# Kernel optimization log

Measured on AMD Instinct MI355X. Metric: run time of the kernel, lower is better.

## Reference

```python
import jax, jax.numpy as jnp
import numpy as np

H = 16        # head_nums
DN = 128      # qk_nope_head_dim
DR = 64       # qk_rope_head_dim
DV = 128      # v_head_dim
QLR = 1536    # q_lora_rank
KVLR = 512    # kv_lora_rank
HID = 2048    # hidden_dim
THETA = 10000.0
EPS = 1e-6


def _rms(x, w):
    return x * jax.lax.rsqrt(jnp.mean(x * x, axis=-1, keepdims=True) + EPS) * w


def _reorder(x):
    # replicates view(b,h,s,d//2,2).transpose(4,3).reshape: [x0,x2,...,x1,x3,...]
    return jnp.concatenate([x[..., 0::2], x[..., 1::2]], axis=-1)


def _rotate_half(x):
    h = x.shape[-1] // 2
    return jnp.concatenate([-x[..., h:], x[..., :h]], axis=-1)


def setup_inputs() -> dict:
    key = jax.random.key(0)
    ks = jax.random.split(key, 7)
    B, S = 1, 2048

    def w(k, i, o):
        return jax.random.normal(k, (i, o), jnp.float32) * (i ** -0.5)

    return {
        "x": jax.random.normal(ks[0], (B, S, HID), jnp.float32),
        "Wq_down": w(ks[1], HID, QLR),
        "q_norm_w": jnp.ones((QLR,), jnp.float32),
        "Wq_up": w(ks[2], QLR, H * (DN + DR)),
        "Wkv_down": w(ks[3], HID, KVLR + DR),
        "kv_norm_w": jnp.ones((KVLR,), jnp.float32),
        "Wkv_up": w(ks[4], KVLR, H * (DN + DV)),
        "Wo": w(ks[5], HID, HID),
        "position": jnp.broadcast_to(jnp.arange(S, dtype=jnp.int32)[None], (B, S)),
        "mask": jnp.tril(jnp.ones((S, S), bool))[None, None],  # causal [1,1,S,S]
    }


def reference(x, Wq_down, q_norm_w, Wq_up, Wkv_down, kv_norm_w, Wkv_up, Wo, position, mask):
    B, S, _ = x.shape
    # low-rank Q path: down-proj -> RMSNorm -> up-proj -> [B,H,S,DN+DR]
    q = _rms(x @ Wq_down, q_norm_w) @ Wq_up
    q = q.reshape(B, S, H, DN + DR).transpose(0, 2, 1, 3)
    q_nope, q_rope = q[..., :DN], q[..., DN:]
    # latent KV path
    ckv = x @ Wkv_down
    c, k_rope = ckv[..., :KVLR], ckv[..., KVLR:]
    c = _rms(c, kv_norm_w)
    kv = (c @ Wkv_up).reshape(B, S, H, DN + DV).transpose(0, 2, 1, 3)
    k_nope, v = kv[..., :DN], kv[..., DN:]
    k_rope = k_rope[:, None]  # [B,1,S,DR] shared across heads
    # rotary tables
    inv_freq = 1.0 / (THETA ** (jnp.arange(0, DR, 2, dtype=jnp.float32) / DR))
    t = jnp.arange(S, dtype=jnp.float32)
    emb = jnp.concatenate([jnp.outer(t, inv_freq)] * 2, axis=-1)  # [S,DR]
    cos = jnp.cos(emb)[position][:, None]  # [B,1,S,DR]
    sin = jnp.sin(emb)[position][:, None]
    qr, kr = _reorder(q_rope), _reorder(k_rope)
    q_rot = qr * cos + _rotate_half(qr) * sin
    k_rot = kr * cos + _rotate_half(kr) * sin
    q_state = jnp.concatenate([q_nope, q_rot], axis=-1)              # [B,H,S,DN+DR]
    k_state = jnp.concatenate(
        [k_nope, jnp.broadcast_to(k_rot, (B, H, S, DR))], axis=-1)   # [B,H,S,DN+DR]
    scores = jnp.einsum('bhsd,bhtd->bhst', q_state, k_state) / np.float32(np.sqrt(DV))
    scores = jnp.where(mask, scores, -jnp.inf)
    att = jax.nn.softmax(scores, axis=-1)
    out = jnp.einsum('bhst,bhtd->bhsd', att, v)
    out = out.transpose(0, 2, 1, 3).reshape(B, S, H * DV)
    return out @ Wo
```

## Files before the change

kernel.cpp:

```cpp
#include <hip/hip_runtime.h>
#include <hip/hip_bf16.h>
#include <cstddef>

#define H 16
#define DN 128
#define DR 64
#define DV 128
#define QLR 1536
#define KVLR 512
#define HID 2048
#define SLEN 2048
#define EPS 1e-6f
#define SCALE 0.08838834764831845f
#define QK_SCALE (0.08838834764831845f * 1.4426950408889634f)

typedef __attribute__((ext_vector_type(8))) short short8;
typedef __attribute__((ext_vector_type(4))) float f32x4;
typedef unsigned short u16;

__device__ __forceinline__ u16 f2bf(float f) {
    __hip_bfloat16 h = __float2bfloat16(f);
    return __builtin_bit_cast(u16, h);
}
__device__ __forceinline__ float b2f(u16 v) {
    return __bfloat162float(__builtin_bit_cast(__hip_bfloat16, v));
}
__device__ __forceinline__ unsigned pack2(float a, float b) {
    return (unsigned)f2bf(a) | ((unsigned)f2bf(b) << 16);
}

__device__ __forceinline__ void tcast_block(
    const float* __restrict__ W, u16* __restrict__ Wt,
    int K, int N, int nx, float scale, int b, float (*T)[65])
{
    const int tid = threadIdx.x;
    const int bx = b % nx, by = b / nx;
    const int n0 = bx * 64, k0 = by * 64;
    const bool inb = (n0 < N);
    {
        int r = tid >> 4, c4 = (tid & 15) * 4;
        #pragma unroll
        for (int rr = 0; rr < 4; ++rr) {
            int row = rr * 16 + r;
            float4 v = inb ? *reinterpret_cast<const float4*>(W + (size_t)(k0 + row) * N + n0 + c4)
                           : make_float4(0.f, 0.f, 0.f, 0.f);
            T[row][c4] = v.x * scale; T[row][c4 + 1] = v.y * scale;
            T[row][c4 + 2] = v.z * scale; T[row][c4 + 3] = v.w * scale;
        }
    }
    __syncthreads();
    {
        int n = tid >> 2, kq = (tid & 3) * 16;
        unsigned u[8];
        #pragma unroll
        for (int jj = 0; jj < 8; ++jj)
            u[jj] = pack2(T[kq + 2 * jj][n], T[kq + 2 * jj + 1][n]);
        u16* dst = Wt + (size_t)(n0 + n) * K + k0 + kq;
        *reinterpret_cast<uint4*>(dst)     = make_uint4(u[0], u[1], u[2], u[3]);
        *reinterpret_cast<uint4*>(dst + 8) = make_uint4(u[4], u[5], u[6], u[7]);
    }
}

__global__ __launch_bounds__(256) void prep_all(
    const float* __restrict__ x, u16* __restrict__ xb,
    const float* __restrict__ Wqd, const float* __restrict__ Wkvd,
    u16* __restrict__ BtF)
{
    const int tid = threadIdx.x;
    if (blockIdx.x < 2048) {
        size_t base = ((size_t)blockIdx.x * 256 + tid) * 8;
        float4 v0 = *reinterpret_cast<const float4*>(x + base);
        float4 v1 = *reinterpret_cast<const float4*>(x + base + 4);
        union { short8 s; unsigned u[4]; } p;
        p.u[0] = pack2(v0.x, v0.y); p.u[1] = pack2(v0.z, v0.w);
        p.u[2] = pack2(v1.x, v1.y); p.u[3] = pack2(v1.z, v1.w);
        *reinterpret_cast<short8*>(xb + base) = p.s;
        return;
    }
    __shared__ float T[64][65];
    int b = blockIdx.x - 2048;
    if (b < 768) tcast_block(Wqd, BtF, 2048, 1536, 24, 1.0f, b, T);
    else         tcast_block(Wkvd, BtF + (size_t)1536 * 2048, 2048, 576, 10, 1.0f, b - 768, T);
}

__device__ __forceinline__ void stage6(const char* const* gb, const unsigned* srcOff,
                                       const int* ldsBase, u16* smemBuf, unsigned koff)
{
    #pragma unroll
    for (int j = 0; j < 6; ++j)
        __builtin_amdgcn_global_load_lds(
            (const __attribute__((address_space(1))) unsigned int*)(gb[j] + srcOff[j] + koff),
            (__attribute__((address_space(3))) unsigned int*)(smemBuf + ldsBase[j]),
            16, 0, 0);
}

template<bool BF16OUT>
__device__ __forceinline__ void gemm_core64(
    const u16* __restrict__ A, const u16* __restrict__ Bt, void* __restrict__ Cv,
    int N, int K, int m0, int n0, u16 (*smem)[12288])
{
    const int tid = threadIdx.x, lane = tid & 63, w = tid >> 6;
    const int colk = lane & 15, grp16 = (lane >> 4) * 16;
    const size_t Kb = (size_t)K * 2;

    const char* gb[6];
    unsigned srcOff[6];
    int ldsBase[6];
    #pragma unroll
    for (int j = 0; j < 6; ++j) {
        int c = w * 6 + j;
        bool isA = (c < 8);
        int cc = isA ? c : c - 8;
        int o = cc * 1024 + lane * 16;
        int u = o ^ (((o >> 7) & 7) << 4);
        int row = u >> 7, kbyte = u & 127;
        gb[j] = isA ? (const char*)A : (const char*)Bt;
        srcOff[j] = (unsigned)((size_t)(isA ? m0 + row : n0 + row) * Kb + kbyte);
        ldsBase[j] = isA ? cc * 512 : 4096 + cc * 512;
    }

    const int wc = w * 32;
    int aoff[8], boff[4];
    #pragma unroll
    for (int ks = 0; ks < 2; ++ks) {
        #pragma unroll
        for (int i = 0; i < 4; ++i) {
            int ra = i * 16 + colk;
            int oa = ra * 128 + ks * 64 + grp16;
            aoff[ks * 4 + i] = oa ^ ((ra & 7) << 4);
        }
        #pragma unroll
        for (int jj = 0; jj < 2; ++jj) {
            int rb = wc + jj * 16 + colk;
            int ob = rb * 128 + ks * 64 + grp16;
            boff[ks * 2 + jj] = (ob ^ ((rb & 7) << 4)) + 8192;
        }
    }

    f32x4 acc[4][2];
    #pragma unroll
    for (int i = 0; i < 4; ++i)
        #pragma unroll
        for (int j = 0; j < 2; ++j) acc[i][j] = (f32x4){0.f, 0.f, 0.f, 0.f};

    const int NT = K >> 6;
    stage6(gb, srcOff, ldsBase, &smem[0][0], 0);
    __syncthreads();
    int cur = 0;
    for (int t = 0; t < NT; ++t) {
        if (t + 1 < NT) stage6(gb, srcOff, ldsBase, &smem[cur ^ 1][0], (unsigned)(t + 1) * 128);
        const char* base = (const char*)&smem[cur][0];
        #pragma unroll
        for (int ks = 0; ks < 2; ++ks) {
            short8 af[4], bfr[2];
            #pragma unroll
            for (int i = 0; i < 4; ++i) af[i] = *reinterpret_cast<const short8*>(base + aoff[ks * 4 + i]);
            #pragma unroll
            for (int jj = 0; jj < 2; ++jj) bfr[jj] = *reinterpret_cast<const short8*>(base + boff[ks * 2 + jj]);
            __builtin_amdgcn_s_setprio(1);
            #pragma unroll
            for (int i = 0; i < 4; ++i)
                #pragma unroll
                for (int jj = 0; jj < 2; ++jj)
                    acc[i][jj] = __builtin_amdgcn_mfma_f32_16x16x32_bf16(af[i], bfr[jj], acc[i][jj], 0, 0, 0);
            __builtin_amdgcn_s_setprio(0);
        }
        __syncthreads();
        cur ^= 1;
    }

    #pragma unroll
    for (int i = 0; i < 4; ++i) {
        int grow0 = m0 + i * 16 + (grp16 >> 2);
        #pragma unroll
        for (int jj = 0; jj < 2; ++jj) {
            int gcol = n0 + wc + jj * 16 + colk;
            if (gcol < N) {
                #pragma unroll
                for (int r = 0; r < 4; ++r) {
                    float v2 = acc[i][jj][r];
                    if (BF16OUT) ((u16*)Cv)[(size_t)(grow0 + r) * N + gcol] = f2bf(v2);
                    else         ((float*)Cv)[(size_t)(grow0 + r) * N + gcol] = v2;
                }
            }
        }
    }
}

__device__ __forceinline__ void xcd_map(int orig, int nwg, int nby, int& bx, int& by)
{
    int xcd = orig & 7, o8 = orig >> 3;
    int qq = nwg >> 3, rr = nwg & 7;
    int v = (xcd < rr ? xcd * (qq + 1) : rr * (qq + 1) + (xcd - rr) * qq) + o8;
    bx = v / nby; by = v - bx * nby;
}

__global__ __launch_bounds__(256) void gemm_down_fused(
    const u16* __restrict__ xb, const u16* __restrict__ BtF, float* __restrict__ fC,
    const float* __restrict__ Wqu, const float* __restrict__ Wkvu, const float* __restrict__ Wo,
    u16* __restrict__ Wqu_t, u16* __restrict__ Wkvu_t, u16* __restrict__ Wo_t)
{
    __shared__ u16 smem[2][12288];
    if (blockIdx.x < 544) {
        int bx, by;
        xcd_map(blockIdx.x, 544, 32, bx, by);
        gemm_core64<false>(xb, BtF, fC, 2112, 2048, by * 64, bx * 128, smem);
        return;
    }
    float (*T)[65] = reinterpret_cast<float(*)[65]>(&smem[0][0]);
    int b = blockIdx.x - 544;
    if (b < 1152)      tcast_block(Wqu,  Wqu_t,  1536, 3072, 48, QK_SCALE, b, T);
    else if (b < 1664) tcast_block(Wkvu, Wkvu_t, 512,  4096, 64, 1.0f, b - 1152, T);
    else               tcast_block(Wo,   Wo_t,   2048, 2048, 32, 1.0f, b - 1664, T);
}

__global__ __launch_bounds__(256) void gemm_dual(
    const u16* __restrict__ Aq, const u16* __restrict__ Bq, u16* __restrict__ Cq,
    const u16* __restrict__ Ak, const u16* __restrict__ Bk, u16* __restrict__ Ck)
{
    __shared__ u16 smem[2][12288];
    int b = blockIdx.x;
    const u16 *A, *Bt; u16* C; int N, K, nwg;
    if (b < 768) { A = Aq; Bt = Bq; C = Cq; N = 3072; K = 1536; nwg = 768; }
    else { b -= 768; A = Ak; Bt = Bk; C = Ck; N = 4096; K = 512; nwg = 1024; }
    int bx, by;
    xcd_map(b, nwg, 32, bx, by);
    gemm_core64<true>(A, Bt, C, N, K, by * 64, bx * 128, smem);
}

__global__ __launch_bounds__(256) void gemm_wo(
    const u16* __restrict__ A, const u16* __restrict__ Bt, float* __restrict__ C)
{
    __shared__ u16 smem[2][12288];
    int bx, by;
    xcd_map(blockIdx.x, 512, 32, bx, by);
    gemm_core64<false>(A, Bt, C, 2048, 2048, by * 64, bx * 128, smem);
}

__global__ __launch_bounds__(256) void rmsnorm2_bf16(
    const float* __restrict__ fC, const float* __restrict__ qw,
    const float* __restrict__ kvw, u16* __restrict__ qdb, u16* __restrict__ ckvb)
{
    const int row = blockIdx.x, tid = threadIdx.x;
    const float* p = fC + (size_t)row * 2112;
    float ssq = 0.f, ssk = 0.f;
    for (int i = tid * 4; i < 1536; i += 1024) {
        float4 v = *reinterpret_cast<const float4*>(p + i);
        ssq += v.x * v.x + v.y * v.y + v.z * v.z + v.w * v.w;
    }
    if (tid < 128) {
        float4 v = *reinterpret_cast<const float4*>(p + 1536 + tid * 4);
        ssk = v.x * v.x + v.y * v.y + v.z * v.z + v.w * v.w;
    }
    __shared__ float wsq[4], wsk[4];
    int lane = tid & 63, wv = tid >> 6;
    #pragma unroll
    for (int off = 32; off; off >>= 1) {
        ssq += __shfl_down(ssq, off);
        ssk += __shfl_down(ssk, off);
    }
    if (lane == 0) { wsq[wv] = ssq; wsk[wv] = ssk; }
    __syncthreads();
    if (tid == 0) {
        wsq[0] = rsqrtf((wsq[0] + wsq[1] + wsq[2] + wsq[3]) / 1536.f + EPS);
        wsk[0] = rsqrtf((wsk[0] + wsk[1] + wsk[2] + wsk[3]) / 512.f + EPS);
    }
    __syncthreads();
    float scq = wsq[0], sck = wsk[0];
    for (int i = tid * 4; i < 1536; i += 1024) {
        float4 v = *reinterpret_cast<const float4*>(p + i);
        float4 g = *reinterpret_cast<const float4*>(qw + i);
        *reinterpret_cast<uint2*>(qdb + (size_t)row * 1536 + i) =
            make_uint2(pack2(v.x * scq * g.x, v.y * scq * g.y),
                       pack2(v.z * scq * g.z, v.w * scq * g.w));
    }
    if (tid < 128) {
        int i = tid * 4;
        float4 v = *reinterpret_cast<const float4*>(p + 1536 + i);
        float4 g = *reinterpret_cast<const float4*>(kvw + i);
        *reinterpret_cast<uint2*>(ckvb + (size_t)row * 512 + i) =
            make_uint2(pack2(v.x * sck * g.x, v.y * sck * g.y),
                       pack2(v.z * sck * g.z, v.w * sck * g.w));
    }
}

__global__ __launch_bounds__(256) void rope_vtrans(
    u16* __restrict__ q, const float* __restrict__ krsrc, int krStride,
    u16* __restrict__ krot, const u16* __restrict__ kvbf, u16* __restrict__ vtb)
{
    const int tid = threadIdx.x;
    if (blockIdx.x < 2048) {
        const int s = blockIdx.x;
        __shared__ float cs[32], sn[32];
        if (tid < 32) {
            float inv = powf(10000.0f, -(float)tid / 32.0f);
            float ang = (float)s * inv;
            cs[tid] = cosf(ang); sn[tid] = sinf(ang);
        }
        __syncthreads();
        float ev[2], ov[2]; int hh[2], ii[2];
        #pragma unroll
        for (int it = 0; it < 2; ++it) {
            int pidx = tid + it * 256;
            int h = pidx >> 5, i = pidx & 31;
            hh[it] = h; ii[it] = i;
            const u16* base = q + (size_t)s * 3072 + h * 192 + 128;
            ev[it] = b2f(base[2 * i]); ov[it] = b2f(base[2 * i + 1]);
        }
        __syncthreads();
        #pragma unroll
        for (int it = 0; it < 2; ++it) {
            int h = hh[it], i = ii[it];
            u16* base = q + (size_t)s * 3072 + h * 192 + 128;
            base[i]      = f2bf(ev[it] * cs[i] - ov[it] * sn[i]);
            base[32 + i] = f2bf(ov[it] * cs[i] + ev[it] * sn[i]);
        }
        if (tid < 32) {
            int i = tid;
            float e = krsrc[(size_t)s * krStride + 2 * i];
            float o = krsrc[(size_t)s * krStride + 2 * i + 1];
            krot[(size_t)s * 64 + i]      = f2bf(e * cs[i] - o * sn[i]);
            krot[(size_t)s * 64 + 32 + i] = f2bf(o * cs[i] + e * sn[i]);
        }
        return;
    }
    const int bid = blockIdx.x - 2048;
    const int h = bid & 15, rem = bid >> 4;
    const int st = rem & 31, dt = rem >> 5;
    __shared__ u16 T[64][72];
    #pragma unroll
    for (int it = 0; it < 2; ++it) {
        int c = it * 256 + tid;
        int r = c >> 3, c8 = (c & 7) * 8;
        short8 v = *reinterpret_cast<const short8*>(
            kvbf + ((size_t)(st * 64 + r) * 16 + h) * 256 + 128 + dt * 64 + c8);
        *reinterpret_cast<short8*>(&T[r][c8]) = v;
    }
    __syncthreads();
    #pragma unroll
    for (int it = 0; it < 2; ++it) {
        int c = it * 256 + tid;
        int d = c >> 3, s8 = (c & 7) * 8;
        union { short8 s; u16 e[8]; } o;
        #pragma unroll
        for (int j = 0; j < 8; ++j) o.e[j] = T[s8 + j][d];
        *reinterpret_cast<short8*>(
            vtb + ((size_t)(h * 128 + dt * 64 + d)) * 2048 + st * 64 + s8) = o.s;
    }
}

__global__ __launch_bounds__(256, 2) void attn_chunk(
    const u16* __restrict__ qbf,
    const u16* __restrict__ kvbf,
    const u16* __restrict__ krot,
    const u16* __restrict__ vtb,
    u16* __restrict__ outb,
    u16* __restrict__ partAcc,
    float* __restrict__ partML)
{
    const int bid = blockIdx.x;
    const int xcd = bid & 7, slot = bid >> 3;
    const int h = xcd + 8 * (slot & 1);
    const int r80 = 79 - (slot >> 1);
    int qb, ch, S, poff;
    if (r80 < 8)       { qb = r80;                 ch = 0;      S = 1; poff = 0; }
    else if (r80 < 24) { int u = r80 - 8;  qb = 8 + (u >> 1);  ch = u & 1; S = 2; poff = (qb - 8) * 2 + ch; }
    else if (r80 < 48) { int u = r80 - 24; qb = 16 + u / 3;    ch = u % 3; S = 3; poff = 16 + (qb - 16) * 3 + ch; }
    else               { int u = r80 - 48; qb = 24 + (u >> 2); ch = u & 3; S = 4; poff = 40 + (qb - 24) * 4 + ch; }
    const int s0 = qb * 64;
    const int t0 = ch * 8;
    const int t1 = (t0 + 8 < qb + 1) ? (t0 + 8) : (qb + 1);
    const int slotId = h * 72 + poff;
    const int tid = threadIdx.x, lane = tid & 63, w = tid >> 6;
    const int colk = lane & 15, grp = lane >> 4, g8 = grp * 8;

    __shared__ u16 Ks[64 * 192];
    __shared__ u16 Vt[128 * 64];

    const int qg = s0 + w * 16 + colk;

    short8 qreg[6];
    {
        const u16* qp = qbf + ((size_t)qg * H + h) * 192;
        #pragma unroll
        for (int ks = 0; ks < 6; ++ks)
            qreg[ks] = *reinterpret_cast<const short8*>(qp + ks * 32 + g8);
    }

    int kt[6], kslot[6];
    #pragma unroll
    for (int it = 0; it < 6; ++it) {
        int c = it * 256 + tid;
        kt[it] = c / 24; kslot[it] = c % 24;
    }
    int vr[4], vks_[4];
    #pragma unroll
    for (int it = 0; it < 4; ++it) {
        int c = it * 256 + tid;
        vr[it] = c >> 3; vks_[it] = c & 7;
    }

    short8 kreg[6], vregV[4];

    auto issue_loads = [&](int t) {
        #pragma unroll
        for (int it = 0; it < 6; ++it) {
            int gk = t * 64 + kt[it];
            const u16* src = (kslot[it] < 16)
                ? kvbf + ((size_t)gk * H + h) * 256 + kslot[it] * 8
                : krot + (size_t)gk * 64 + (kslot[it] - 16) * 8;
            kreg[it] = *reinterpret_cast<const short8*>(src);
        }
        const u16* vT = vtb + (size_t)h * 128 * 2048 + t * 64;
        #pragma unroll
        for (int it = 0; it < 4; ++it)
            vregV[it] = *reinterpret_cast<const short8*>(
                vT + (size_t)vr[it] * 2048 + vks_[it] * 8);
    };
    auto write_lds = [&]() {
        #pragma unroll
        for (int it = 0; it < 6; ++it) {
            int sl = (kslot[it] & 24) | ((kslot[it] ^ kt[it]) & 7);
            *reinterpret_cast<short8*>(&Ks[kt[it] * 192 + sl * 8]) = kreg[it];
        }
        #pragma unroll
        for (int it = 0; it < 4; ++it)
            *reinterpret_cast<short8*>(
                &Vt[vr[it] * 64 + ((vks_[it] ^ vr[it]) & 7) * 8]) = vregV[it];
    };

    float m_run = -1e30f, l_run = 0.f;
    f32x4 acc_o[8];
    #pragma unroll
    for (int i = 0; i < 8; ++i) acc_o[i] = (f32x4){0.f, 0.f, 0.f, 0.f};

    const int srcA = colk + ((grp & 1) << 5);
    const int srcB = srcA + 16;
    const bool hiSel = (grp >> 1) != 0;

    issue_loads(t0);
    for (int t = t0; t < t1; ++t) {
        __syncthreads();
        write_lds();
        __syncthreads();
        if (t + 1 < t1) issue_loads(t + 1);

        f32x4 sacc[4];
        #pragma unroll
        for (int ct = 0; ct < 4; ++ct) sacc[ct] = (f32x4){0.f, 0.f, 0.f, 0.f};
        __builtin_amdgcn_s_setprio(1);
        #pragma unroll
        for (int ks = 0; ks < 6; ++ks) {
            #pragma unroll
            for (int ct = 0; ct < 4; ++ct) {
                int key = ct * 16 + colk;
                int slotIdx = ks * 4 + grp;
                int sl = (slotIdx & 24) | ((slotIdx ^ key) & 7);
                short8 kf = *reinterpret_cast<const short8*>(&Ks[key * 192 + sl * 8]);
                sacc[ct] = __builtin_amdgcn_mfma_f32_16x16x32_bf16(kf, qreg[ks], sacc[ct], 0, 0, 0);
            }
        }
        __builtin_amdgcn_s_setprio(0);

        if (t == qb) {
            #pragma unroll
            for (int ct = 0; ct < 4; ++ct) {
                int keyb = t * 64 + ct * 16 + 4 * grp;
                #pragma unroll
                for (int r = 0; r < 4; ++r)
                    if (keyb + r > qg) sacc[ct][r] = -1e30f;
            }
        }

        float lmax = fmaxf(fmaxf(fmaxf(sacc[0][0], sacc[0][1]), fmaxf(sacc[0][2], sacc[0][3])),
                           fmaxf(fmaxf(sacc[1][0], sacc[1][1]), fmaxf(sacc[1][2], sacc[1][3])));
        lmax = fmaxf(lmax,
               fmaxf(fmaxf(fmaxf(sacc[2][0], sacc[2][1]), fmaxf(sacc[2][2], sacc[2][3])),
                     fmaxf(fmaxf(sacc[3][0], sacc[3][1]), fmaxf(sacc[3][2], sacc[3][3]))));
        bool need = lmax > m_run + 11.5f;
        if (__any((int)need)) {
            float mx = fmaxf(m_run, lmax);
            mx = fmaxf(mx, __shfl_xor(mx, 16));
            mx = fmaxf(mx, __shfl_xor(mx, 32));
            float f = exp2f(m_run - mx);
            m_run = mx;
            l_run *= f;
            #pragma unroll
            for (int i = 0; i < 8; ++i) {
                acc_o[i][0] *= f; acc_o[i][1] *= f;
                acc_o[i][2] *= f; acc_o[i][3] *= f;
            }
        }

        unsigned pku[8];
        float psum = 0.f;
        #pragma unroll
        for (int ct = 0; ct < 4; ++ct) {
            float p0 = exp2f(sacc[ct][0] - m_run);
            float p1 = exp2f(sacc[ct][1] - m_run);
            float p2 = exp2f(sacc[ct][2] - m_run);
            float p3 = exp2f(sacc[ct][3] - m_run);
            psum += (p0 + p1) + (p2 + p3);
            pku[ct * 2]     = pack2(p0, p1);
            pku[ct * 2 + 1] = pack2(p2, p3);
        }
        l_run += psum;

        __builtin_amdgcn_s_setprio(1);
        #pragma unroll
        for (int ks2 = 0; ks2 < 2; ++ks2) {
            unsigned a0 = __shfl(pku[4 * ks2 + 0], srcA);
            unsigned a1 = __shfl(pku[4 * ks2 + 1], srcA);
            unsigned a2 = __shfl(pku[4 * ks2 + 0], srcB);
            unsigned a3 = __shfl(pku[4 * ks2 + 1], srcB);
            unsigned b0 = __shfl(pku[4 * ks2 + 2], srcA);
            unsigned b1 = __shfl(pku[4 * ks2 + 3], srcA);
            unsigned b2 = __shfl(pku[4 * ks2 + 2], srcB);
            unsigned b3 = __shfl(pku[4 * ks2 + 3], srcB);
            union { short8 s; unsigned u[4]; } bq;
            bq.u[0] = hiSel ? b0 : a0;
            bq.u[1] = hiSel ? b1 : a1;
            bq.u[2] = hiSel ? b2 : a2;
            bq.u[3] = hiSel ? b3 : a3;
            #pragma unroll
            for (int ct = 0; ct < 8; ++ct) {
                int cc = ct * 16 + colk;
                int vsl = ((ks2 * 4 + grp) ^ cc) & 7;
                short8 vb = *reinterpret_cast<const short8*>(&Vt[cc * 64 + vsl * 8]);
                acc_o[ct] = __builtin_amdgcn_mfma_f32_16x16x32_bf16(vb, bq.s, acc_o[ct], 0, 0, 0);
            }
        }
        __builtin_amdgcn_s_setprio(0);
    }

    float l = l_run;
    l += __shfl_xor(l, 16);
    l += __shfl_xor(l, 32);
    const int rloc = w * 16 + colk;
    if (S == 1) {
        float invl = 1.0f / l;
        u16* orow = outb + (size_t)qg * 2048 + h * 128 + 4 * grp;
        #pragma unroll
        for (int ct = 0; ct < 8; ++ct) {
            uint2 pk;
            pk.x = pack2(acc_o[ct][0] * invl, acc_o[ct][1] * invl);
            pk.y = pack2(acc_o[ct][2] * invl, acc_o[ct][3] * invl);
            *reinterpret_cast<uint2*>(orow + ct * 16) = pk;
        }
    } else {
        if (grp == 0) {
            partML[(size_t)slotId * 128 + rloc * 2]     = m_run;
            partML[(size_t)slotId * 128 + rloc * 2 + 1] = l;
        }
        u16* pa = partAcc + (size_t)slotId * 8192 + rloc * 128 + 4 * grp;
        #pragma unroll
        for (int ct = 0; ct < 8; ++ct) {
            uint2 pk;
            pk.x = pack2(acc_o[ct][0], acc_o[ct][1]);
            pk.y = pack2(acc_o[ct][2], acc_o[ct][3]);
            *reinterpret_cast<uint2*>(pa + ct * 16) = pk;
        }
    }
}

__global__ __launch_bounds__(256) void attn_combine(
    const u16* __restrict__ partAcc, const float* __restrict__ partML,
    u16* __restrict__ outb)
{
    const int bid = blockIdx.x;
    const int xcd = bid & 7, s2 = bid >> 3;
    const int h = xcd + 8 * (s2 / 24);
    const int qb = 8 + s2 % 24;
    int S, poff;
    if (qb < 16)      { S = 2; poff = (qb - 8) * 2; }
    else if (qb < 24) { S = 3; poff = 16 + (qb - 16) * 3; }
    else              { S = 4; poff = 40 + (qb - 24) * 4; }
    const int base = h * 72 + poff;
    const int tid = threadIdx.x;
    const int row = tid >> 2, seg = (tid & 3) * 32;

    float mv[4], lv[4];
    float m_g = -1e30f;
    #pragma unroll
    for (int s = 0; s < 4; ++s) {
        bool ok = (s < S);
        mv[s] = ok ? partML[(size_t)(base + s) * 128 + row * 2]     : -1e30f;
        lv[s] = ok ? partML[(size_t)(base + s) * 128 + row * 2 + 1] : 0.f;
        m_g = fmaxf(m_g, mv[s]);
    }
    float l_g = 0.f, wq[4];
    #pragma unroll
    for (int s = 0; s < 4; ++s) { wq[s] = exp2f(mv[s] - m_g); l_g += wq[s] * lv[s]; }
    float inv = 1.f / l_g;
    u16* orow = outb + (size_t)(qb * 64 + row) * 2048 + h * 128 + seg;
    #pragma unroll
    for (int i = 0; i < 8; ++i) {
        float o[4] = {0.f, 0.f, 0.f, 0.f};
        #pragma unroll
        for (int s = 0; s < 4; ++s) {
            if (s < S) {
                ushort4 a = *reinterpret_cast<const ushort4*>(
                    partAcc + (size_t)(base + s) * 8192 + row * 128 + seg + i * 4);
                o[0] += wq[s] * b2f(a.x); o[1] += wq[s] * b2f(a.y);
                o[2] += wq[s] * b2f(a.z); o[3] += wq[s] * b2f(a.w);
            }
        }
        uint2 pk;
        pk.x = pack2(o[0] * inv, o[1] * inv);
        pk.y = pack2(o[2] * inv, o[3] * inv);
        *reinterpret_cast<uint2*>(orow + i * 4) = pk;
    }
}

extern "C" void kernel_launch(void* const* d_in, const int* in_sizes, int n_in,
                              void* d_out, int out_size, void* d_ws, size_t ws_size,
                              hipStream_t stream)
{
    (void)in_sizes; (void)n_in; (void)out_size; (void)ws_size;
    const float* x         = (const float*)d_in[0];
    const float* Wq_down   = (const float*)d_in[1];
    const float* q_norm_w  = (const float*)d_in[2];
    const float* Wq_up     = (const float*)d_in[3];
    const float* Wkv_down  = (const float*)d_in[4];
    const float* kv_norm_w = (const float*)d_in[5];
    const float* Wkv_up    = (const float*)d_in[6];
    const float* Wo        = (const float*)d_in[7];
    float* out = (float*)d_out;

    char* p = (char*)d_ws;
    u16* BtF     = (u16*)p;   p += (size_t)2176 * 2048 * 2;
    u16* Wkvu_t  = (u16*)p;   p += (size_t)4096 * 512  * 2;
    u16* Wo_t    = (u16*)p;   p += (size_t)2048 * 2048 * 2;
    u16* qbuf    = (u16*)p;   p += (size_t)2048 * 3072 * 2;
    u16* ckvb    = (u16*)p;   p += (size_t)2048 * 512  * 2;
    u16* kvbf    = (u16*)p;   p += (size_t)2048 * 4096 * 2;
    u16* krotb   = (u16*)p;   p += (size_t)2048 * 64   * 2;
    char* pool   = p;
    u16* xb      = (u16*)p;   p += (size_t)2048 * 2048 * 2;
    u16* Wqu_t   = (u16*)p;   p += (size_t)3072 * 1536 * 2;
    float* fC    = (float*)p; p += (size_t)2048 * 2112 * 4;
    u16* qdb     = (u16*)p;   p += (size_t)2048 * 1536 * 2;
    u16* attb    = (u16*)BtF;
    u16* partAcc = xb;
    float* partML  = (float*)(partAcc + (size_t)1152 * 8192);
    u16* vtb     = (u16*)(pool + (size_t)20 * 1024 * 1024);

    dim3 blk(256);
    prep_all<<<3136, blk, 0, stream>>>(x, xb, Wq_down, Wkv_down, BtF);

    gemm_down_fused<<<3232, blk, 0, stream>>>(xb, BtF, fC, Wq_up, Wkv_up, Wo,
                                              Wqu_t, Wkvu_t, Wo_t);
    rmsnorm2_bf16<<<2048, blk, 0, stream>>>(fC, q_norm_w, kv_norm_w, qdb, ckvb);
    gemm_dual<<<dim3(1792), blk, 0, stream>>>(qdb, Wqu_t, qbuf, ckvb, Wkvu_t, kvbf);
    rope_vtrans<<<3072, blk, 0, stream>>>(qbuf, fC + 2048, 2112, krotb, kvbf, vtb);

    attn_chunk<<<dim3(1280), blk, 0, stream>>>(qbuf, kvbf, krotb, vtb, attb, partAcc, partML);
    attn_combine<<<dim3(384), blk, 0, stream>>>(partAcc, partML, attb);

    gemm_wo<<<dim3(512), blk, 0, stream>>>(attb, Wo_t, out);
}
```

Measured before the change: 187.7 us.

## Double-buffer attention KV tiles via direct global-to-LDS loads with 32-key tiles

The attention kernel now streams K and V tiles straight from global memory into LDS with global_load_lds, bypassing the register staging copy. Two LDS buffers allow the next tile's load to overlap compute on the current one. Each tile shrinks from 64 keys to 32, which keeps the double buffer within a similar LDS budget and uses a new swizzle. Only one barrier per iteration remains, but there are twice as many iterations, and the smaller tiles give less MFMA work per barrier and per softmax step.

```diff
diff --git a/kernel.cpp b/kernel.cpp
--- a/kernel.cpp
+++ b/kernel.cpp
@@ -368,14 +368,14 @@
     else if (r80 < 48) { int u = r80 - 24; qb = 16 + u / 3;    ch = u % 3; S = 3; poff = 16 + (qb - 16) * 3 + ch; }
     else               { int u = r80 - 48; qb = 24 + (u >> 2); ch = u & 3; S = 4; poff = 40 + (qb - 24) * 4 + ch; }
     const int s0 = qb * 64;
-    const int t0 = ch * 8;
-    const int t1 = (t0 + 8 < qb + 1) ? (t0 + 8) : (qb + 1);
+    const int nt32 = 2 * qb + 2;
+    const int t0 = ch * 16;
+    const int t1 = (t0 + 16 < nt32) ? (t0 + 16) : nt32;
     const int slotId = h * 72 + poff;
     const int tid = threadIdx.x, lane = tid & 63, w = tid >> 6;
     const int colk = lane & 15, grp = lane >> 4, g8 = grp * 8;
 
-    __shared__ u16 Ks[64 * 192];
-    __shared__ u16 Vt[128 * 64];
+    __shared__ u16 smem[2][10240];
 
     const int qg = s0 + w * 16 + colk;
 
@@ -387,47 +387,38 @@
             qreg[ks] = *reinterpret_cast<const short8*>(qp + ks * 32 + g8);
     }
 
-    int kt[6], kslot[6];
-    #pragma unroll
-    for (int it = 0; it < 6; ++it) {
-        int c = it * 256 + tid;
-        kt[it] = c / 24; kslot[it] = c % 24;
-    }
-    int vr[4], vks_[4];
-    #pragma unroll
-    for (int it = 0; it < 4; ++it) {
-        int c = it * 256 + tid;
-        vr[it] = c >> 3; vks_[it] = c & 7;
-    }
-
-    short8 kreg[6], vregV[4];
-
-    auto issue_loads = [&](int t) {
-        #pragma unroll
-        for (int it = 0; it < 6; ++it) {
-            int gk = t * 64 + kt[it];
-            const u16* src = (kslot[it] < 16)
-                ? kvbf + ((size_t)gk * H + h) * 256 + kslot[it] * 8
-                : krot + (size_t)gk * 64 + (kslot[it] - 16) * 8;
-            kreg[it] = *reinterpret_cast<const short8*>(src);
-        }
-        const u16* vT = vtb + (size_t)h * 128 * 2048 + t * 64;
-        #pragma unroll
-        for (int it = 0; it < 4; ++it)
-            vregV[it] = *reinterpret_cast<const short8*>(
-                vT + (size_t)vr[it] * 2048 + vks_[it] * 8);
-    };
-    auto write_lds = [&]() {
-        #pragma unroll
-        for (int it = 0; it < 6; ++it) {
-            int sl = (kslot[it] & 24) | ((kslot[it] ^ kt[it]) & 7);
-            *reinterpret_cast<short8*>(&Ks[kt[it] * 192 + sl * 8]) = kreg[it];
-        }
-        #pragma unroll
-        for (int it = 0; it < 4; ++it)
-            *reinterpret_cast<short8*>(
-                &Vt[vr[it] * 64 + ((vks_[it] ^ vr[it]) & 7) * 8]) = vregV[it];
-    };
+    const char* gbase[5];
+    unsigned curOff[5], strideB[5];
+    int ldsOff[5];
+    #pragma unroll
+    for (int j = 0; j < 5; ++j) {
+        int c = w * 5 + j;
+        if (c < 12) {
+            int o = c * 1024 + lane * 16;
+            int row = o / 384, rem = o % 384, s = rem >> 4;
+            int kslot = (s & 24) | ((s ^ row) & 7);
+            if (kslot < 16) {
+                gbase[j] = (const char*)(kvbf + h * 256);
+                curOff[j] = (unsigned)((row * 4096 + kslot * 8) * 2);
+                strideB[j] = 32 * 4096 * 2;
+            } else {
+                gbase[j] = (const char*)krot;
+                curOff[j] = (unsigned)((row * 64 + (kslot - 16) * 8) * 2);
+                strideB[j] = 32 * 64 * 2;
+            }
+            ldsOff[j] = c * 512;
+        } else {
+            int cc = c - 12;
+            int o = cc * 1024 + lane * 16;
+            int row = o >> 6, s = (o & 63) >> 4;
+            int vks = (s ^ row ^ (row >> 2)) & 3;
+            gbase[j] = (const char*)(vtb + (size_t)h * 128 * 2048);
+            curOff[j] = (unsigned)((row * 2048 + vks * 8) * 2);
+            strideB[j] = 32 * 2;
+            ldsOff[j] = 6144 + cc * 512;
+        }
+        curOff[j] += (unsigned)t0 * strideB[j];
+    }
 
     float m_run = -1e30f, l_run = 0.f;
     f32x4 acc_o[8];
@@ -438,34 +429,53 @@
     const int srcB = srcA + 16;
     const bool hiSel = (grp >> 1) != 0;
 
-    issue_loads(t0);
+    #pragma unroll
+    for (int j = 0; j < 5; ++j) {
+        __builtin_amdgcn_global_load_lds(
+            (const __attribute__((address_space(1))) unsigned int*)(gbase[j] + curOff[j]),
+            (__attribute__((address_space(3))) unsigned int*)(&smem[0][0] + ldsOff[j]),
+            16, 0, 0);
+        curOff[j] += strideB[j];
+    }
+    __syncthreads();
+
+    int buf = 0;
     for (int t = t0; t < t1; ++t) {
-        __syncthreads();
-        write_lds();
-        __syncthreads();
-        if (t + 1 < t1) issue_loads(t + 1);
-
-        f32x4 sacc[4];
-        #pragma unroll
-        for (int ct = 0; ct < 4; ++ct) sacc[ct] = (f32x4){0.f, 0.f, 0.f, 0.f};
+        if (t + 1 < t1) {
+            u16* dst = &smem[buf ^ 1][0];
+            #pragma unroll
+            for (int j = 0; j < 5; ++j) {
+                __builtin_amdgcn_global_load_lds(
+                    (const __attribute__((address_space(1))) unsigned int*)(gbase[j] + curOff[j]),
+                    (__attribute__((address_space(3))) unsigned int*)(dst + ldsOff[j]),
+                    16, 0, 0);
+                curOff[j] += strideB[j];
+            }
+        }
+        const u16* KsB = &smem[buf][0];
+        const u16* VtB = &smem[buf][6144];
+
+        f32x4 sacc[2];
+        sacc[0] = (f32x4){0.f, 0.f, 0.f, 0.f};
+        sacc[1] = (f32x4){0.f, 0.f, 0.f, 0.f};
         __builtin_amdgcn_s_setprio(1);
         #pragma unroll
         for (int ks = 0; ks < 6; ++ks) {
             #pragma unroll
-            for (int ct = 0; ct < 4; ++ct) {
+            for (int ct = 0; ct < 2; ++ct) {
                 int key = ct * 16 + colk;
                 int slotIdx = ks * 4 + grp;
                 int sl = (slotIdx & 24) | ((slotIdx ^ key) & 7);
-                short8 kf = *reinterpret_cast<const short8*>(&Ks[key * 192 + sl * 8]);
+                short8 kf = *reinterpret_cast<const short8*>(&KsB[key * 192 + sl * 8]);
                 sacc[ct] = __builtin_amdgcn_mfma_f32_16x16x32_bf16(kf, qreg[ks], sacc[ct], 0, 0, 0);
             }
         }
         __builtin_amdgcn_s_setprio(0);
 
-        if (t == qb) {
+        if (t >= 2 * qb) {
             #pragma unroll
-            for (int ct = 0; ct < 4; ++ct) {
-                int keyb = t * 64 + ct * 16 + 4 * grp;
+            for (int ct = 0; ct < 2; ++ct) {
+                int keyb = t * 32 + ct * 16 + 4 * grp;
                 #pragma unroll
                 for (int r = 0; r < 4; ++r)
                     if (keyb + r > qg) sacc[ct][r] = -1e30f;
@@ -474,9 +484,6 @@
 
         float lmax = fmaxf(fmaxf(fmaxf(sacc[0][0], sacc[0][1]), fmaxf(sacc[0][2], sacc[0][3])),
                            fmaxf(fmaxf(sacc[1][0], sacc[1][1]), fmaxf(sacc[1][2], sacc[1][3])));
-        lmax = fmaxf(lmax,
-               fmaxf(fmaxf(fmaxf(sacc[2][0], sacc[2][1]), fmaxf(sacc[2][2], sacc[2][3])),
-                     fmaxf(fmaxf(sacc[3][0], sacc[3][1]), fmaxf(sacc[3][2], sacc[3][3]))));
         bool need = lmax > m_run + 11.5f;
         if (__any((int)need)) {
             float mx = fmaxf(m_run, lmax);
@@ -492,10 +499,10 @@
             }
         }
 
-        unsigned pku[8];
+        unsigned pku[4];
         float psum = 0.f;
         #pragma unroll
-        for (int ct = 0; ct < 4; ++ct) {
+        for (int ct = 0; ct < 2; ++ct) {
             float p0 = exp2f(sacc[ct][0] - m_run);
             float p1 = exp2f(sacc[ct][1] - m_run);
             float p2 = exp2f(sacc[ct][2] - m_run);
@@ -506,31 +513,31 @@
         }
         l_run += psum;
 
+        unsigned a0 = __shfl(pku[0], srcA);
+        unsigned a1 = __shfl(pku[1], srcA);
+        unsigned a2 = __shfl(pku[0], srcB);
+        unsigned a3 = __shfl(pku[1], srcB);
+        unsigned b0 = __shfl(pku[2], srcA);
+        unsigned b1 = __shfl(pku[3], srcA);
+        unsigned b2 = __shfl(pku[2], srcB);
+        unsigned b3 = __shfl(pku[3], srcB);
+        union { short8 s; unsigned u[4]; } bq;
+        bq.u[0] = hiSel ? b0 : a0;
+        bq.u[1] = hiSel ? b1 : a1;
+        bq.u[2] = hiSel ? b2 : a2;
+        bq.u[3] = hiSel ? b3 : a3;
         __builtin_amdgcn_s_setprio(1);
         #pragma unroll
-        for (int ks2 = 0; ks2 < 2; ++ks2) {
-            unsigned a0 = __shfl(pku[4 * ks2 + 0], srcA);
-            unsigned a1 = __shfl(pku[4 * ks2 + 1], srcA);
-            unsigned a2 = __shfl(pku[4 * ks2 + 0], srcB);
-            unsigned a3 = __shfl(pku[4 * ks2 + 1], srcB);
-            unsigned b0 = __shfl(pku[4 * ks2 + 2], srcA);
-            unsigned b1 = __shfl(pku[4 * ks2 + 3], srcA);
-            unsigned b2 = __shfl(pku[4 * ks2 + 2], srcB);
-            unsigned b3 = __shfl(pku[4 * ks2 + 3], srcB);
-            union { short8 s; unsigned u[4]; } bq;
-            bq.u[0] = hiSel ? b0 : a0;
-            bq.u[1] = hiSel ? b1 : a1;
-            bq.u[2] = hiSel ? b2 : a2;
-            bq.u[3] = hiSel ? b3 : a3;
-            #pragma unroll
-            for (int ct = 0; ct < 8; ++ct) {
-                int cc = ct * 16 + colk;
-                int vsl = ((ks2 * 4 + grp) ^ cc) & 7;
-                short8 vb = *reinterpret_cast<const short8*>(&Vt[cc * 64 + vsl * 8]);
-                acc_o[ct] = __builtin_amdgcn_mfma_f32_16x16x32_bf16(vb, bq.s, acc_o[ct], 0, 0, 0);
-            }
+        for (int ct = 0; ct < 8; ++ct) {
+            int cc = ct * 16 + colk;
+            int vsl = (grp ^ cc ^ (cc >> 2)) & 3;
+            short8 vb = *reinterpret_cast<const short8*>(&VtB[cc * 32 + vsl * 8]);
+            acc_o[ct] = __builtin_amdgcn_mfma_f32_16x16x32_bf16(vb, bq.s, acc_o[ct], 0, 0, 0);
         }
         __builtin_amdgcn_s_setprio(0);
+
+        __syncthreads();
+        buf ^= 1;
     }
 
     float l = l_run;
```

New measurement: 184.3 us, median of 2. About the same (-1.8%).
